# Optimization experiments

Measured on AMD Instinct MI355X. Metric: run time of the kernel, lower is better.

The kernel has to match this reference:

```python
import jax, jax.numpy as jnp
import numpy as np

B, S, E, H = 2, 2048, 1024, 16
HD = E // H


def setup_inputs() -> dict:
    key = jax.random.key(0)
    ks = jax.random.split(key, 9)
    s = 1.0 / np.sqrt(E)
    return {
        "x": jax.random.normal(ks[0], (B, S, E), dtype=jnp.float32),
        "wq": jax.random.uniform(ks[1], (E, E), jnp.float32, -s, s),
        "bq": jax.random.uniform(ks[2], (E,), jnp.float32, -s, s),
        "wk": jax.random.uniform(ks[3], (E, E), jnp.float32, -s, s),
        "bk": jax.random.uniform(ks[4], (E,), jnp.float32, -s, s),
        "wv": jax.random.uniform(ks[5], (E, E), jnp.float32, -s, s),
        "bv": jax.random.uniform(ks[6], (E,), jnp.float32, -s, s),
        "wo": jax.random.uniform(ks[7], (E, E), jnp.float32, -s, s),
        "bo": jax.random.uniform(ks[8], (E,), jnp.float32, -s, s),
    }


def reference(x, wq, bq, wk, bk, wv, bv, wo, bo):
    b, s, e = x.shape
    # QKV projections, reshape to [b, h, s, hd]
    def proj(w, bias):
        y = jnp.einsum('bse,ef->bsf', x, w.T) + bias
        return y.reshape(b, s, H, HD).transpose(0, 2, 1, 3)
    q = proj(wq, bq)
    k = proj(wk, bk)
    v = proj(wv, bv)
    score = jnp.einsum('bhqd,bhkd->bhqk', q, k) / jnp.sqrt(jnp.float32(HD))
    # original: exp(x)/sum(exp(x)) + 1e-8  == softmax(x) + 1e-8
    attn = jax.nn.softmax(score, axis=-1) + 1e-8
    out = jnp.einsum('bhqk,bhkd->bhqd', attn, v)
    out = out.transpose(0, 2, 1, 3).reshape(b, s, e)
    return jnp.einsum('bse,ef->bsf', out, wo.T) + bo
```

## Files before the change

### kernel.cpp

```cpp
#include <hip/hip_runtime.h>
#include <hip/hip_bf16.h>
#include <cstdint>

#define SS 2048
#define EE 1024
#define HH 16
#define HDD 64

typedef __attribute__((ext_vector_type(8))) __bf16 bf16x8;
typedef __attribute__((ext_vector_type(4))) float f32x4;

#define MFMA16(a, b, c) __builtin_amdgcn_mfma_f32_16x16x32_bf16((a), (b), (c), 0, 0, 0)

__device__ __forceinline__ unsigned short f2bf(float f) {
    unsigned int u = __builtin_bit_cast(unsigned int, f);
    u += 0x7FFFu + ((u >> 16) & 1u);
    return (unsigned short)(u >> 16);
}

__device__ __forceinline__ void gll16(const unsigned short* g, unsigned short* l) {
    __builtin_amdgcn_global_load_lds(
        (__attribute__((address_space(1))) unsigned int*)g,
        (__attribute__((address_space(3))) unsigned int*)l, 16, 0, 0);
}

__global__ __launch_bounds__(256) void cvt_all(
    const float* __restrict__ x, const float* __restrict__ wq, const float* __restrict__ wk,
    const float* __restrict__ wv, const float* __restrict__ wo,
    unsigned short* __restrict__ xb, unsigned short* __restrict__ wqb, unsigned short* __restrict__ wkb,
    unsigned short* __restrict__ wvb, unsigned short* __restrict__ wob) {
    int idx = blockIdx.x * 256 + threadIdx.x;
    int i4 = idx << 2;
    const float* src;
    unsigned short* dst;
    int off;
    if (i4 < 4194304) { src = x; dst = xb; off = i4; }
    else {
        int w = (i4 - 4194304) >> 20;
        off = (i4 - 4194304) & 1048575;
        if (w == 0) { src = wq; dst = wqb; }
        else if (w == 1) { src = wk; dst = wkb; }
        else if (w == 2) { src = wv; dst = wvb; }
        else { src = wo; dst = wob; }
    }
    float4 v = *(const float4*)&src[off];
    unsigned int p0 = (unsigned int)f2bf(v.x) | ((unsigned int)f2bf(v.y) << 16);
    unsigned int p1 = (unsigned int)f2bf(v.z) | ((unsigned int)f2bf(v.w) << 16);
    uint2 u; u.x = p0; u.y = p1;
    *(uint2*)&dst[off] = u;
}

template <int MODE, int BMT, int BNT>
__device__ __forceinline__ void gemm_core(
    unsigned short* __restrict__ lsA,
    unsigned short* __restrict__ lsB,
    const unsigned short* __restrict__ A, const unsigned short* __restrict__ W,
    const float* __restrict__ bias, void* __restrict__ out, int bm, int bn) {
    constexpr int IT = BMT / 32, JT = BNT / 32;
    constexpr int ASTR = BMT * 32, BSTR = BNT * 32;
    const int t = threadIdx.x;
    const int lane = t & 63, l15 = lane & 15, quad = lane >> 4;
    const int wave = t >> 6;
    const int wm = (wave >> 1) * (BMT / 2), wn = (wave & 1) * (BNT / 2);

    const int cg = ((t & 3) ^ ((t >> 3) & 3)) * 8;
    const unsigned short* ga = A + (size_t)(bm + (t >> 2)) * 1024 + cg;
    const unsigned short* gb = W + (size_t)(bn + (t >> 2)) * 1024 + cg;

    f32x4 acc[IT][JT];
    for (int i = 0; i < IT; i++)
        for (int j = 0; j < JT; j++) acc[i][j] = (f32x4){0.f, 0.f, 0.f, 0.f};

    const int swz = (l15 >> 1) & 3;

    gll16(ga, &lsA[t * 8]);
    if (BMT == 128) gll16(ga + 64 * 1024, &lsA[2048 + t * 8]);
    gll16(gb, &lsB[t * 8]);
    if (BNT == 128) gll16(gb + 64 * 1024, &lsB[2048 + t * 8]);

    for (int it = 0; it < 32; it++) {
        const int cur = it & 1, nxt = cur ^ 1;
        __syncthreads();

        if (it < 31) {
            const int k0 = (it + 1) * 32;
            gll16(ga + k0, &lsA[nxt * ASTR + t * 8]);
            if (BMT == 128) gll16(ga + k0 + 64 * 1024, &lsA[nxt * ASTR + 2048 + t * 8]);
            gll16(gb + k0, &lsB[nxt * BSTR + t * 8]);
            if (BNT == 128) gll16(gb + k0 + 64 * 1024, &lsB[nxt * BSTR + 2048 + t * 8]);
        }

        bf16x8 af[IT], bfr[JT];
        for (int i = 0; i < IT; i++)
            af[i] = *(const bf16x8*)&lsA[cur * ASTR + (wm + i * 16 + l15) * 32 + ((quad ^ swz) * 8)];
        for (int j = 0; j < JT; j++)
            bfr[j] = *(const bf16x8*)&lsB[cur * BSTR + (wn + j * 16 + l15) * 32 + ((quad ^ swz) * 8)];
        for (int i = 0; i < IT; i++)
            for (int j = 0; j < JT; j++) acc[i][j] = MFMA16(af[i], bfr[j], acc[i][j]);
    }

    for (int j = 0; j < JT; j++) {
        int n = bn + wn + j * 16 + l15;
        float bj = bias[n];
        for (int i = 0; i < IT; i++) {
            int m0 = bm + wm + i * 16 + quad * 4;
            int srow0 = m0 & 2047, bidx = m0 >> 11;
            if (MODE == 3) {
                size_t headb = ((size_t)bidx * HH + (n >> 6)) * (SS * HDD);
                size_t base = headb + (size_t)(srow0 >> 6) * 4096 +
                              (size_t)(((srow0 >> 4) & 3) * 8 + ((n & 63) >> 3)) * 128 + (n & 7);
                for (int rg = 0; rg < 4; rg++)
                    ((unsigned short*)out)[base + (size_t)((srow0 & 15) + rg) * 8] = f2bf(acc[i][j][rg] + bj);
            } else if (MODE == 4) {
                size_t headb = ((size_t)bidx * HH + (n >> 6)) * (SS * HDD);
                size_t addr = headb + (size_t)(srow0 >> 6) * 4096 + (size_t)((n & 63) >> 4) * 1024 +
                              (size_t)(((srow0 >> 5) & 1) * 4 + ((srow0 >> 3) & 3)) * 128 +
                              (size_t)(n & 15) * 8 + (srow0 & 7);
                float v0 = acc[i][j][0] + bj, v1 = acc[i][j][1] + bj;
                float v2 = acc[i][j][2] + bj, v3 = acc[i][j][3] + bj;
                uint2 w;
                w.x = (unsigned int)f2bf(v0) | ((unsigned int)f2bf(v1) << 16);
                w.y = (unsigned int)f2bf(v2) | ((unsigned int)f2bf(v3) << 16);
                *(uint2*)&((unsigned short*)out)[addr] = w;
            } else {
                for (int rg = 0; rg < 4; rg++) {
                    float val = acc[i][j][rg] + bj;
                    int m = m0 + rg;
                    if (MODE == 0) {
                        ((unsigned short*)out)[(((size_t)(m >> 11) * HH + (n >> 6)) * SS + (m & 2047)) * HDD + (n & 63)] = f2bf(val);
                    } else {
                        ((float*)out)[(size_t)m * 1024 + n] = val;
                    }
                }
            }
        }
    }
}

__global__ __launch_bounds__(256) void gemm_qkv(
    const unsigned short* __restrict__ xb,
    const unsigned short* __restrict__ wqb, const unsigned short* __restrict__ wkb,
    const unsigned short* __restrict__ wvb,
    const float* __restrict__ bq, const float* __restrict__ bk, const float* __restrict__ bv,
    unsigned short* qb, unsigned short* kb, unsigned short* vtb) {
    __shared__ unsigned short shA[2 * 4096];
    __shared__ unsigned short shB[2 * 4096];
    const int blk = blockIdx.x;
    const int u = blk & 7, r = blk >> 3;
    const int by = u + 8 * (r & 3);
    const int rest = r >> 2;
    const int bx = rest & 7, z = rest >> 3;
    if (z == 0)      gemm_core<0, 128, 128>(shA, shB, xb, wqb, bq, qb,  by * 128, bx * 128);
    else if (z == 1) gemm_core<3, 128, 128>(shA, shB, xb, wkb, bk, kb,  by * 128, bx * 128);
    else             gemm_core<4, 128, 128>(shA, shB, xb, wvb, bv, vtb, by * 128, bx * 128);
}

__global__ __launch_bounds__(256) void gemm_out(
    const unsigned short* __restrict__ ob, const unsigned short* __restrict__ wob,
    const float* __restrict__ bo, float* __restrict__ out) {
    __shared__ unsigned short shA[2 * 4096];
    __shared__ unsigned short shB[2 * 2048];
    const int blk = blockIdx.x;
    const int u = blk & 7, r = blk >> 3;
    const int by = u + 8 * (r & 3);
    const int bx = r >> 2;
    gemm_core<1, 128, 64>(shA, shB, ob, wob, bo, out, by * 128, bx * 64);
}

#define PSTR 72

__global__ __launch_bounds__(512, 4) void attn_fwd(
    const unsigned short* __restrict__ qb, const unsigned short* __restrict__ kb,
    const unsigned short* __restrict__ vtb, unsigned short* __restrict__ ob) {
    __shared__ unsigned short sh[8192 + 8192 + 8 * 32 * PSTR];
    unsigned short* lsK = sh;
    unsigned short* lsV = sh + 8192;
    unsigned short* lsP = sh + 16384;
    const int t = threadIdx.x, lane = t & 63, l15 = lane & 15, quad = lane >> 4;
    const int wave = t >> 6;
    const int half = wave >> 2;
    const int wq = wave & 3;
    const int tg = t & 255;
    const int blk = blockIdx.x;
    const int u = blk & 7, r = blk >> 3;
    const int bh = u + 8 * (r & 3);
    const int qt = r >> 2;
    const size_t hoff = (size_t)bh * (SS * HDD);
    const float C = 0.125f * 1.44269504088896f;

    bf16x8 qf[2][2];
    const int qrow = qt * 128 + wq * 32;
    for (int i = 0; i < 2; i++)
        for (int ks = 0; ks < 2; ks++) {
            bf16x8 raw = *(const bf16x8*)&qb[hoff + (size_t)(qrow + i * 16 + l15) * HDD + ks * 32 + quad * 8];
            unsigned short tmp[8];
            *(bf16x8*)tmp = raw;
            for (int j = 0; j < 8; j++) {
                float f = __builtin_bit_cast(float, (unsigned int)tmp[j] << 16);
                tmp[j] = f2bf(f * C);
            }
            qf[i][ks] = *(const bf16x8*)tmp;
        }

    unsigned short onesbuf[8];
    for (int j = 0; j < 8; j++) onesbuf[j] = 0x3F80;
    const bf16x8 onesf = *(const bf16x8*)onesbuf;

    f32x4 lacc[2];
    f32x4 o[2][4];
    for (int i = 0; i < 2; i++) {
        lacc[i] = (f32x4){0.f, 0.f, 0.f, 0.f};
        for (int jh = 0; jh < 4; jh++) o[i][jh] = (f32x4){0.f, 0.f, 0.f, 0.f};
    }

    const unsigned short* gk = kb + hoff + (size_t)half * 16 * 4096;
    const unsigned short* gv = vtb + hoff + (size_t)half * 16 * 4096;
    unsigned short* myK = lsK + half * 4096;
    unsigned short* myV = lsV + half * 4096;
    const int pbase = wave * 32 * PSTR;
    const int foff = quad * 128 + l15 * 8;

    gll16(gk + tg * 8, myK + tg * 8);
    gll16(gk + 2048 + tg * 8, myK + 2048 + tg * 8);
    gll16(gv + tg * 8, myV + tg * 8);
    gll16(gv + 2048 + tg * 8, myV + 2048 + tg * 8);

    for (int kt = 0; kt < 16; kt++) {
        __syncthreads();

        bf16x8 kfr[4][2];
        for (int j = 0; j < 4; j++)
            for (int ks = 0; ks < 2; ks++)
                kfr[j][ks] = *(const bf16x8*)&myK[j * 1024 + ks * 512 + foff];

        f32x4 st[4][2];
        for (int j = 0; j < 4; j++)
            for (int i = 0; i < 2; i++) {
                f32x4 z = (f32x4){0.f, 0.f, 0.f, 0.f};
                z = MFMA16(kfr[j][0], qf[i][0], z);
                z = MFMA16(kfr[j][1], qf[i][1], z);
                st[j][i] = z;
            }

        for (int j = 0; j < 4; j++)
            for (int i = 0; i < 2; i++) {
                float e0 = __builtin_amdgcn_exp2f(st[j][i][0]);
                float e1 = __builtin_amdgcn_exp2f(st[j][i][1]);
                float e2 = __builtin_amdgcn_exp2f(st[j][i][2]);
                float e3 = __builtin_amdgcn_exp2f(st[j][i][3]);
                uint2 w;
                w.x = (__builtin_bit_cast(unsigned int, e0) >> 16) |
                      (__builtin_bit_cast(unsigned int, e1) & 0xFFFF0000u);
                w.y = (__builtin_bit_cast(unsigned int, e2) >> 16) |
                      (__builtin_bit_cast(unsigned int, e3) & 0xFFFF0000u);
                *(uint2*)&lsP[pbase + (i * 16 + l15) * PSTR + j * 16 + quad * 4] = w;
            }

        bf16x8 pf[2][2], vf[4][2];
        for (int i = 0; i < 2; i++)
            for (int ks = 0; ks < 2; ks++)
                pf[i][ks] = *(const bf16x8*)&lsP[pbase + (i * 16 + l15) * PSTR + ks * 32 + quad * 8];
        for (int jh = 0; jh < 4; jh++)
            for (int ks = 0; ks < 2; ks++)
                vf[jh][ks] = *(const bf16x8*)&myV[jh * 1024 + ks * 512 + foff];
        for (int i = 0; i < 2; i++) {
            for (int jh = 0; jh < 4; jh++) {
                o[i][jh] = MFMA16(pf[i][0], vf[jh][0], o[i][jh]);
                o[i][jh] = MFMA16(pf[i][1], vf[jh][1], o[i][jh]);
            }
            lacc[i] = MFMA16(pf[i][0], onesf, lacc[i]);
            lacc[i] = MFMA16(pf[i][1], onesf, lacc[i]);
        }

        if (kt < 15) {
            __syncthreads();
            const unsigned short* gkn = gk + (kt + 1) * 4096;
            const unsigned short* gvn = gv + (kt + 1) * 4096;
            gll16(gkn + tg * 8, myK + tg * 8);
            gll16(gkn + 2048 + tg * 8, myK + 2048 + tg * 8);
            gll16(gvn + tg * 8, myV + tg * 8);
            gll16(gvn + 2048 + tg * 8, myV + 2048 + tg * 8);
        }
    }

    __syncthreads();
    float* cb = (float*)sh;
    float* lb = cb + 8192;
    const int lslot = wq * 64 + lane;
    if (half == 1) {
        for (int i = 0; i < 2; i++)
            for (int jh = 0; jh < 4; jh++)
                for (int rg = 0; rg < 4; rg++)
                    cb[(i * 16 + jh * 4 + rg) * 256 + lslot] = o[i][jh][rg];
        for (int i = 0; i < 2; i++)
            for (int rg = 0; rg < 4; rg++)
                lb[(i * 4 + rg) * 256 + lslot] = lacc[i][rg];
    }
    __syncthreads();
    if (half == 0) {
        const int b = bh >> 4, h = bh & 15;
        for (int i = 0; i < 2; i++)
            for (int rg = 0; rg < 4; rg++) {
                float inv = 1.f / (lacc[i][rg] + lb[(i * 4 + rg) * 256 + lslot]);
                int srow = qrow + i * 16 + quad * 4 + rg;
                size_t rowoff = ((size_t)b * SS + srow) * EE + h * 64;
                for (int jh = 0; jh < 4; jh++) {
                    float val = o[i][jh][rg] + cb[(i * 16 + jh * 4 + rg) * 256 + lslot];
                    ob[rowoff + jh * 16 + l15] = f2bf(val * inv);
                }
            }
    }
}

extern "C" void kernel_launch(void* const* d_in, const int* in_sizes, int n_in,
                              void* d_out, int out_size, void* d_ws, size_t ws_size,
                              hipStream_t stream) {
    const float* x  = (const float*)d_in[0];
    const float* wq = (const float*)d_in[1];
    const float* bq = (const float*)d_in[2];
    const float* wk = (const float*)d_in[3];
    const float* bk = (const float*)d_in[4];
    const float* wv = (const float*)d_in[5];
    const float* bv = (const float*)d_in[6];
    const float* wo = (const float*)d_in[7];
    const float* bo = (const float*)d_in[8];

    char* ws = (char*)d_ws;
    unsigned short* xb  = (unsigned short*)(ws + 0);
    unsigned short* wqb = (unsigned short*)(ws + 8388608);
    unsigned short* wkb = (unsigned short*)(ws + 10485760);
    unsigned short* wvb = (unsigned short*)(ws + 12582912);
    unsigned short* wob = (unsigned short*)(ws + 14680064);
    unsigned short* qb  = (unsigned short*)(ws + 16777216);
    unsigned short* kb  = (unsigned short*)(ws + 25165824);
    unsigned short* vtb = (unsigned short*)(ws + 33554432);
    unsigned short* ob  = xb;

    cvt_all<<<8192, 256, 0, stream>>>(x, wq, wk, wv, wo, xb, wqb, wkb, wvb, wob);
    gemm_qkv<<<768, 256, 0, stream>>>(xb, wqb, wkb, wvb, bq, bk, bv, qb, kb, vtb);
    attn_fwd<<<512, 512, 0, stream>>>(qb, kb, vtb, ob);
    gemm_out<<<512, 256, 0, stream>>>(ob, wob, bo, (float*)d_out);
}
```

Baseline: 188.4 us.

## Keep attention probabilities in registers via permlane swaps instead of LDS round-trip

The softmax numerators are no longer written to shared memory and read back as MFMA operands. They are rearranged in registers with permlane32/permlane16 swaps, which removes the P staging buffer and its LDS traffic. Row sums are now accumulated with scalar adds and cross-lane shuffles instead of extra MFMAs against a ones vector. The smaller LDS footprint lets the occupancy hint rise from 4 to 6 blocks, at the cost of more VALU work and a correctness dependence on the lane mapping of the swaps.

```diff
diff --git a/kernel.cpp b/kernel.cpp
--- a/kernel.cpp
+++ b/kernel.cpp
@@ -18,10 +18,38 @@
     return (unsigned short)(u >> 16);
 }
 
+__device__ __forceinline__ float bcf(unsigned int u) {
+    return __builtin_bit_cast(float, u);
+}
+
 __device__ __forceinline__ void gll16(const unsigned short* g, unsigned short* l) {
     __builtin_amdgcn_global_load_lds(
         (__attribute__((address_space(1))) unsigned int*)g,
         (__attribute__((address_space(3))) unsigned int*)l, 16, 0, 0);
+}
+
+__device__ __forceinline__ void pl32swap(unsigned int& a, unsigned int& b) {
+#if __has_builtin(__builtin_amdgcn_permlane32_swap)
+    auto r = __builtin_amdgcn_permlane32_swap(a, b, false, false);
+    a = r[0]; b = r[1];
+#else
+    unsigned int as = __shfl_xor(a, 32, 64), bs = __shfl_xor(b, 32, 64);
+    const bool hi = (threadIdx.x & 32) != 0;
+    unsigned int na = hi ? bs : a, nb = hi ? b : as;
+    a = na; b = nb;
+#endif
+}
+
+__device__ __forceinline__ void pl16swap(unsigned int& a, unsigned int& b) {
+#if __has_builtin(__builtin_amdgcn_permlane16_swap)
+    auto r = __builtin_amdgcn_permlane16_swap(a, b, false, false);
+    a = r[0]; b = r[1];
+#else
+    unsigned int as = __shfl_xor(a, 16, 64), bs = __shfl_xor(b, 16, 64);
+    const bool odd = (threadIdx.x & 16) != 0;
+    unsigned int na = odd ? bs : a, nb = odd ? b : as;
+    a = na; b = nb;
+#endif
 }
 
 __global__ __launch_bounds__(256) void cvt_all(
@@ -167,15 +195,12 @@
     gemm_core<1, 128, 64>(shA, shB, ob, wob, bo, out, by * 128, bx * 64);
 }
 
-#define PSTR 72
-
-__global__ __launch_bounds__(512, 4) void attn_fwd(
+__global__ __launch_bounds__(512, 6) void attn_fwd(
     const unsigned short* __restrict__ qb, const unsigned short* __restrict__ kb,
     const unsigned short* __restrict__ vtb, unsigned short* __restrict__ ob) {
-    __shared__ unsigned short sh[8192 + 8192 + 8 * 32 * PSTR];
+    __shared__ unsigned short sh[20480];
     unsigned short* lsK = sh;
     unsigned short* lsV = sh + 8192;
-    unsigned short* lsP = sh + 16384;
     const int t = threadIdx.x, lane = t & 63, l15 = lane & 15, quad = lane >> 4;
     const int wave = t >> 6;
     const int half = wave >> 2;
@@ -202,22 +227,15 @@
             qf[i][ks] = *(const bf16x8*)tmp;
         }
 
-    unsigned short onesbuf[8];
-    for (int j = 0; j < 8; j++) onesbuf[j] = 0x3F80;
-    const bf16x8 onesf = *(const bf16x8*)onesbuf;
-
-    f32x4 lacc[2];
     f32x4 o[2][4];
-    for (int i = 0; i < 2; i++) {
-        lacc[i] = (f32x4){0.f, 0.f, 0.f, 0.f};
+    float ps[2] = {0.f, 0.f};
+    for (int i = 0; i < 2; i++)
         for (int jh = 0; jh < 4; jh++) o[i][jh] = (f32x4){0.f, 0.f, 0.f, 0.f};
-    }
 
     const unsigned short* gk = kb + hoff + (size_t)half * 16 * 4096;
     const unsigned short* gv = vtb + hoff + (size_t)half * 16 * 4096;
     unsigned short* myK = lsK + half * 4096;
     unsigned short* myV = lsV + half * 4096;
-    const int pbase = wave * 32 * PSTR;
     const int foff = quad * 128 + l15 * 8;
 
     gll16(gk + tg * 8, myK + tg * 8);
@@ -233,43 +251,58 @@
             for (int ks = 0; ks < 2; ks++)
                 kfr[j][ks] = *(const bf16x8*)&myK[j * 1024 + ks * 512 + foff];
 
-        f32x4 st[4][2];
+        f32x4 st[2][4];
         for (int j = 0; j < 4; j++)
             for (int i = 0; i < 2; i++) {
                 f32x4 z = (f32x4){0.f, 0.f, 0.f, 0.f};
                 z = MFMA16(kfr[j][0], qf[i][0], z);
                 z = MFMA16(kfr[j][1], qf[i][1], z);
-                st[j][i] = z;
-            }
-
-        for (int j = 0; j < 4; j++)
+                st[i][j] = z;
+            }
+
+        bf16x8 pf[2][2];
+        for (int i = 0; i < 2; i++) {
+            unsigned int W[4][2];
+            float accp = 0.f;
+            for (int j = 0; j < 4; j++) {
+                float e0 = __builtin_amdgcn_exp2f(st[i][j][0]);
+                float e1 = __builtin_amdgcn_exp2f(st[i][j][1]);
+                float e2 = __builtin_amdgcn_exp2f(st[i][j][2]);
+                float e3 = __builtin_amdgcn_exp2f(st[i][j][3]);
+                unsigned int w0 = (__builtin_bit_cast(unsigned int, e0) >> 16) |
+                                  (__builtin_bit_cast(unsigned int, e1) & 0xFFFF0000u);
+                unsigned int w1 = (__builtin_bit_cast(unsigned int, e2) >> 16) |
+                                  (__builtin_bit_cast(unsigned int, e3) & 0xFFFF0000u);
+                W[j][0] = w0; W[j][1] = w1;
+                accp += (bcf(w0 << 16) + bcf(w0 & 0xFFFF0000u)) +
+                        (bcf(w1 << 16) + bcf(w1 & 0xFFFF0000u));
+            }
+            ps[i] += accp;
+
+            unsigned int P0[4], P1[4];
+            for (int h = 0; h < 2; h++) {
+                unsigned int x = W[0][h], y = W[1][h];
+                pl32swap(x, y);
+                pl16swap(x, y);
+                P0[h] = x; P0[2 + h] = y;
+                unsigned int x2 = W[2][h], y2 = W[3][h];
+                pl32swap(x2, y2);
+                pl16swap(x2, y2);
+                P1[h] = x2; P1[2 + h] = y2;
+            }
+            union { unsigned int u4[4]; bf16x8 v; } cv0, cv1;
+            for (int p = 0; p < 4; p++) { cv0.u4[p] = P0[p]; cv1.u4[p] = P1[p]; }
+            pf[i][0] = cv0.v;
+            pf[i][1] = cv1.v;
+        }
+
+        for (int jh = 0; jh < 4; jh++) {
+            bf16x8 v0 = *(const bf16x8*)&myV[jh * 1024 + foff];
+            bf16x8 v1 = *(const bf16x8*)&myV[jh * 1024 + 512 + foff];
             for (int i = 0; i < 2; i++) {
-                float e0 = __builtin_amdgcn_exp2f(st[j][i][0]);
-                float e1 = __builtin_amdgcn_exp2f(st[j][i][1]);
-                float e2 = __builtin_amdgcn_exp2f(st[j][i][2]);
-                float e3 = __builtin_amdgcn_exp2f(st[j][i][3]);
-                uint2 w;
-                w.x = (__builtin_bit_cast(unsigned int, e0) >> 16) |
-                      (__builtin_bit_cast(unsigned int, e1) & 0xFFFF0000u);
-                w.y = (__builtin_bit_cast(unsigned int, e2) >> 16) |
-                      (__builtin_bit_cast(unsigned int, e3) & 0xFFFF0000u);
-                *(uint2*)&lsP[pbase + (i * 16 + l15) * PSTR + j * 16 + quad * 4] = w;
-            }
-
-        bf16x8 pf[2][2], vf[4][2];
-        for (int i = 0; i < 2; i++)
-            for (int ks = 0; ks < 2; ks++)
-                pf[i][ks] = *(const bf16x8*)&lsP[pbase + (i * 16 + l15) * PSTR + ks * 32 + quad * 8];
-        for (int jh = 0; jh < 4; jh++)
-            for (int ks = 0; ks < 2; ks++)
-                vf[jh][ks] = *(const bf16x8*)&myV[jh * 1024 + ks * 512 + foff];
-        for (int i = 0; i < 2; i++) {
-            for (int jh = 0; jh < 4; jh++) {
-                o[i][jh] = MFMA16(pf[i][0], vf[jh][0], o[i][jh]);
-                o[i][jh] = MFMA16(pf[i][1], vf[jh][1], o[i][jh]);
-            }
-            lacc[i] = MFMA16(pf[i][0], onesf, lacc[i]);
-            lacc[i] = MFMA16(pf[i][1], onesf, lacc[i]);
+                o[i][jh] = MFMA16(pf[i][0], v0, o[i][jh]);
+                o[i][jh] = MFMA16(pf[i][1], v1, o[i][jh]);
+            }
         }
 
         if (kt < 15) {
@@ -281,6 +314,15 @@
             gll16(gvn + tg * 8, myV + tg * 8);
             gll16(gvn + 2048 + tg * 8, myV + 2048 + tg * 8);
         }
+    }
+
+    float mysum[2][4];
+    for (int i = 0; i < 2; i++) {
+        float xv = ps[i];
+        xv += __shfl_xor(xv, 16, 64);
+        xv += __shfl_xor(xv, 32, 64);
+        for (int rg = 0; rg < 4; rg++)
+            mysum[i][rg] = __shfl(xv, quad * 20 + rg, 64);
     }
 
     __syncthreads();
@@ -294,14 +336,14 @@
                     cb[(i * 16 + jh * 4 + rg) * 256 + lslot] = o[i][jh][rg];
         for (int i = 0; i < 2; i++)
             for (int rg = 0; rg < 4; rg++)
-                lb[(i * 4 + rg) * 256 + lslot] = lacc[i][rg];
+                lb[(i * 4 + rg) * 256 + lslot] = mysum[i][rg];
     }
     __syncthreads();
     if (half == 0) {
         const int b = bh >> 4, h = bh & 15;
         for (int i = 0; i < 2; i++)
             for (int rg = 0; rg < 4; rg++) {
-                float inv = 1.f / (lacc[i][rg] + lb[(i * 4 + rg) * 256 + lslot]);
+                float inv = 1.f / (mysum[i][rg] + lb[(i * 4 + rg) * 256 + lslot]);
                 int srow = qrow + i * 16 + quad * 4 + rg;
                 size_t rowoff = ((size_t)b * SS + srow) * EE + h * 64;
                 for (int jh = 0; jh < 4; jh++) {
```

Measured after the change: 254.2 us. 1.35x slower.
